# Kernel tuning notes

Measured on AMD Instinct MI355X. Metric: run time of the kernel, lower is better.

## Reference

```python
import jax, jax.numpy as jnp
import numpy as np

DIM_MODEL = 512
HEADS = 8
DIM_HEAD = 64
HIDDEN = HEADS * DIM_HEAD
SCALE = DIM_HEAD ** -0.5
GN_EPS = 1e-5


def setup_inputs() -> dict:
    key = jax.random.key(0)
    ks = jax.random.split(key, 7)
    b, t = 8, 4096
    x = jax.random.normal(ks[0], (b, DIM_MODEL, t), dtype=jnp.float32)
    mask = jax.random.randint(ks[1], (b, t), 0, 2) == 1  # bool padding mask
    # 1x1 convs are plain channel matmuls; kernels squeezed to 2D
    w_qkv = jax.random.normal(ks[2], (3 * HIDDEN, DIM_MODEL), dtype=jnp.float32) * (DIM_MODEL ** -0.5)
    w_out = jax.random.normal(ks[3], (DIM_MODEL, HIDDEN), dtype=jnp.float32) * (HIDDEN ** -0.5)
    b_out = jax.random.normal(ks[4], (DIM_MODEL,), dtype=jnp.float32) * 0.01
    gn_gamma = jnp.ones((DIM_MODEL,), dtype=jnp.float32)
    gn_beta = jnp.zeros((DIM_MODEL,), dtype=jnp.float32)
    return {"x": x, "mask": mask, "w_qkv": w_qkv, "w_out": w_out,
            "b_out": b_out, "gn_gamma": gn_gamma, "gn_beta": gn_beta}


def reference(x, mask, w_qkv, w_out, b_out, gn_gamma, gn_beta):
    b, c, t = x.shape
    # to_qkv: 1x1 conv == channel matmul -> [b, 3*hidden, t]
    qkv = jnp.einsum('oc,bct->bot', w_qkv, x)
    q, k, v = jnp.split(qkv, 3, axis=1)
    # 'b (h d) t -> b h d t'
    q = q.reshape(b, HEADS, DIM_HEAD, t)
    k = k.reshape(b, HEADS, DIM_HEAD, t)
    v = v.reshape(b, HEADS, DIM_HEAD, t)
    # additive mask: 0.0 where True, 1e-12 where False; broadcast 'b t -> b 1 1 t'
    maskf = jnp.where(mask, 0.0, 1e-12)[:, None, None, :].astype(x.dtype)
    q = jax.nn.softmax(q, axis=-2) * SCALE            # softmax over feature dim d
    k = jax.nn.softmax(k + maskf, axis=-1)            # softmax over time dim t
    # linear attention: O(t * d * e)
    context = jnp.einsum('bhdn,bhen->bhde', k, v)      # [b, h, d, e]
    out = jnp.einsum('bhde,bhdn->bhen', context, q)    # [b, h, e, t]
    out = out.reshape(b, HIDDEN, t)                    # 'b h e t -> b (h e) t'
    # to_out: 1x1 conv with bias, then GroupNorm(1, dim_model)
    y = jnp.einsum('oc,bct->bot', w_out, out) + b_out[None, :, None]
    mu = jnp.mean(y, axis=(1, 2), keepdims=True)
    var = jnp.var(y, axis=(1, 2), keepdims=True)
    y = (y - mu) * jax.lax.rsqrt(var + GN_EPS)
    return y * gn_gamma[None, :, None] + gn_beta[None, :, None]
```

## Files before the change

kernel.cpp:

```cpp
#include <hip/hip_runtime.h>
#include <stdint.h>

typedef unsigned short u16;
using f32x4 = __attribute__((ext_vector_type(4))) float;
using s16x8 = __attribute__((ext_vector_type(8))) short;

#define MFMA_BF16(a, b, c) __builtin_amdgcn_mfma_f32_16x16x32_bf16((a), (b), (c), 0, 0, 0)

#define GLOAD_LDS16(gptr, lptr)                                                               \
  __builtin_amdgcn_global_load_lds((const __attribute__((address_space(1))) uint32_t*)(gptr), \
                                   (__attribute__((address_space(3))) uint32_t*)(lptr), 16, 0, 0)

__device__ __forceinline__ u16 f2bf(float f) {
  union { float f; uint32_t u; } v; v.f = f;
  uint32_t r = v.u + 0x7fffu + ((v.u >> 16) & 1u);
  return (u16)(r >> 16);
}
__device__ __forceinline__ float bf2f(u16 h) {
  union { uint32_t u; float f; } v; v.u = ((uint32_t)h) << 16;
  return v.f;
}

__global__ void k_transpose_x(const float* __restrict__ x, u16* __restrict__ xT,
                              const float* __restrict__ wq, const float* __restrict__ wo,
                              u16* __restrict__ wqb, u16* __restrict__ wob) {
  if (blockIdx.z == 8) {
    const int nq = 1536 * 512 / 4;
    const int no = 512 * 512 / 4;
    int bid = blockIdx.y * 64 + blockIdx.x;
#pragma unroll
    for (int rep = 0; rep < 2; ++rep) {
      int i = bid * 256 + threadIdx.x + rep * 131072;
      if (i < nq) {
        float4 v = ((const float4*)wq)[i];
        u16* o = wqb + i * 4;
        o[0] = f2bf(v.x); o[1] = f2bf(v.y); o[2] = f2bf(v.z); o[3] = f2bf(v.w);
      } else if (i < nq + no) {
        int j = i - nq;
        float4 v = ((const float4*)wo)[j];
        u16* o = wob + j * 4;
        o[0] = f2bf(v.x); o[1] = f2bf(v.y); o[2] = f2bf(v.z); o[3] = f2bf(v.w);
      }
    }
    return;
  }
  __shared__ u16 tile[64][68];
  int b = blockIdx.z, c0 = blockIdx.y * 64, t0 = blockIdx.x * 64;
  const float* xp = x + ((size_t)b * 512 + c0) * 4096 + t0;
#pragma unroll
  for (int it = 0; it < 4; ++it) {
    int r = it * 16 + (threadIdx.x >> 4), c4 = (threadIdx.x & 15) * 4;
    float4 v = *(const float4*)(xp + (size_t)r * 4096 + c4);
    tile[r][c4 + 0] = f2bf(v.x);
    tile[r][c4 + 1] = f2bf(v.y);
    tile[r][c4 + 2] = f2bf(v.z);
    tile[r][c4 + 3] = f2bf(v.w);
  }
  __syncthreads();
  u16* op = xT + ((size_t)b * 4096 + t0) * 512 + c0;
#pragma unroll
  for (int it = 0; it < 2; ++it) {
    int tr = it * 32 + (threadIdx.x >> 3), cb = (threadIdx.x & 7) * 8;
    s16x8 o;
#pragma unroll
    for (int jj = 0; jj < 8; ++jj) o[jj] = tile[cb + jj][tr];
    *(s16x8*)(op + (size_t)tr * 512 + cb) = o;
  }
}

#define STAGE_A16(u, ktile, bf)                                                        \
  { int L = (u)*512 + tid; int r = L >> 3, pc = L & 7; int lc = pc ^ (r & 7);          \
    GLOAD_LDS16(Ab + (size_t)r * 512 + (ktile) * 64 + lc * 8,                          \
                ((char*)AL) + (bf) * 32768 + (size_t)L * 16); }
#define STAGE_B16(u, ktile, bf)                                                        \
  { int L = (u)*512 + tid; int r = L >> 3, pc = L & 7; int lc = pc ^ (r & 7);          \
    GLOAD_LDS16(BSRCX(r, ktile, lc),                                                   \
                ((char*)BL) + (bf) * 32768 + (size_t)L * 16); }

#define GEMM256_CORE()                                                                 \
  s16x8* AL = (s16x8*)lds;                                                             \
  s16x8* BL = (s16x8*)(lds + 65536);                                                   \
  int tid = threadIdx.x, w = tid >> 6, lane = tid & 63;                                \
  int wr = w >> 2, wc = w & 3;                                                         \
  int hi = lane >> 4, lo = lane & 15;                                                  \
  f32x4 acc[8][4] = {};                                                                \
  _Pragma("unroll")                                                                    \
  for (int u = 0; u < 4; ++u) STAGE_A16(u, 0, 0);                                      \
  _Pragma("unroll")                                                                    \
  for (int u = 0; u < 4; ++u) STAGE_B16(u, 0, 0);                                      \
  asm volatile("s_waitcnt vmcnt(0)" ::: "memory");                                     \
  __syncthreads();                                                                     \
  int cur = 0;                                                                         \
  _Pragma("unroll 2")                                                                  \
  for (int kt = 0; kt < 8; ++kt) {                                                     \
    const s16x8* Ac = AL + cur * 2048;                                                 \
    const s16x8* Bc = BL + cur * 2048;                                                 \
    int nxt = cur ^ 1;                                                                 \
    bool pf = (kt < 7);                                                                \
    s16x8 af[4][2], b0[2][2], b1[2][2];                                                \
    _Pragma("unroll")                                                                  \
    for (int mi = 0; mi < 4; ++mi) {                                                   \
      int r = wr * 128 + mi * 16 + lo;                                                 \
      _Pragma("unroll")                                                                \
      for (int kk = 0; kk < 2; ++kk) {                                                 \
        int lc = kk * 4 + hi;                                                          \
        af[mi][kk] = Ac[r * 8 + (lc ^ (r & 7))];                                       \
      }                                                                                \
    }                                                                                  \
    _Pragma("unroll")                                                                  \
    for (int ni = 0; ni < 2; ++ni) {                                                   \
      int r = wc * 64 + ni * 16 + lo;                                                  \
      _Pragma("unroll")                                                                \
      for (int kk = 0; kk < 2; ++kk) {                                                 \
        int lc = kk * 4 + hi;                                                          \
        b0[ni][kk] = Bc[r * 8 + (lc ^ (r & 7))];                                       \
      }                                                                                \
    }                                                                                  \
    if (pf) { STAGE_A16(0, kt + 1, nxt); STAGE_A16(1, kt + 1, nxt); }                  \
    __builtin_amdgcn_s_setprio(1);                                                     \
    _Pragma("unroll")                                                                  \
    for (int mi = 0; mi < 4; ++mi)                                                     \
      _Pragma("unroll")                                                                \
      for (int ni = 0; ni < 2; ++ni)                                                   \
        _Pragma("unroll")                                                              \
        for (int kk = 0; kk < 2; ++kk)                                                 \
          acc[mi][ni] = MFMA_BF16(af[mi][kk], b0[ni][kk], acc[mi][ni]);                \
    __builtin_amdgcn_s_setprio(0);                                                     \
    _Pragma("unroll")                                                                  \
    for (int ni = 0; ni < 2; ++ni) {                                                   \
      int r = wc * 64 + (ni + 2) * 16 + lo;                                            \
      _Pragma("unroll")                                                                \
      for (int kk = 0; kk < 2; ++kk) {                                                 \
        int lc = kk * 4 + hi;                                                          \
        b1[ni][kk] = Bc[r * 8 + (lc ^ (r & 7))];                                       \
      }                                                                                \
    }                                                                                  \
    if (pf) { STAGE_A16(2, kt + 1, nxt); STAGE_A16(3, kt + 1, nxt); }                  \
    __builtin_amdgcn_s_setprio(1);                                                     \
    _Pragma("unroll")                                                                  \
    for (int mi = 0; mi < 4; ++mi)                                                     \
      _Pragma("unroll")                                                                \
      for (int ni = 0; ni < 2; ++ni)                                                   \
        _Pragma("unroll")                                                              \
        for (int kk = 0; kk < 2; ++kk)                                                 \
          acc[mi][ni + 2] = MFMA_BF16(af[mi][kk], b1[ni][kk], acc[mi][ni + 2]);        \
    __builtin_amdgcn_s_setprio(0);                                                     \
    _Pragma("unroll")                                                                  \
    for (int mi = 0; mi < 4; ++mi) {                                                   \
      int r = wr * 128 + 64 + mi * 16 + lo;                                            \
      _Pragma("unroll")                                                                \
      for (int kk = 0; kk < 2; ++kk) {                                                 \
        int lc = kk * 4 + hi;                                                          \
        af[mi][kk] = Ac[r * 8 + (lc ^ (r & 7))];                                       \
      }                                                                                \
    }                                                                                  \
    if (pf) { STAGE_B16(0, kt + 1, nxt); STAGE_B16(1, kt + 1, nxt); }                  \
    __builtin_amdgcn_s_setprio(1);                                                     \
    _Pragma("unroll")                                                                  \
    for (int mi = 0; mi < 4; ++mi)                                                     \
      _Pragma("unroll")                                                                \
      for (int ni = 0; ni < 2; ++ni)                                                   \
        _Pragma("unroll")                                                              \
        for (int kk = 0; kk < 2; ++kk)                                                 \
          acc[mi + 4][ni + 2] = MFMA_BF16(af[mi][kk], b1[ni][kk], acc[mi + 4][ni + 2]);\
    __builtin_amdgcn_s_setprio(0);                                                     \
    if (pf) { STAGE_B16(2, kt + 1, nxt); STAGE_B16(3, kt + 1, nxt); }                  \
    __builtin_amdgcn_s_setprio(1);                                                     \
    _Pragma("unroll")                                                                  \
    for (int mi = 0; mi < 4; ++mi)                                                     \
      _Pragma("unroll")                                                                \
      for (int ni = 0; ni < 2; ++ni)                                                   \
        _Pragma("unroll")                                                              \
        for (int kk = 0; kk < 2; ++kk)                                                 \
          acc[mi + 4][ni] = MFMA_BF16(af[mi][kk], b0[ni][kk], acc[mi + 4][ni]);        \
    __builtin_amdgcn_s_setprio(0);                                                     \
    asm volatile("s_waitcnt vmcnt(0)" ::: "memory");                                   \
    __syncthreads();                                                                   \
    cur = nxt;                                                                         \
  }

#define BSRCX(r, ktile, lc) (Bb + (size_t)(r) * 512 + (ktile) * 64 + (lc) * 8)
__launch_bounds__(512, 2)
__global__ void k_gemm_qkv(const u16* __restrict__ A, const u16* __restrict__ BT,
                           u16* __restrict__ C, u16* __restrict__ qT,
                           float* __restrict__ spart) {
  extern __shared__ char lds[];
  int b = blockIdx.z;
  int m0 = blockIdx.y * 256, n0 = blockIdx.x * 256;
  const u16* Ab = A + (size_t)m0 * 512;
  const u16* Bb = BT + ((size_t)b * 4096 + n0) * 512;
  GEMM256_CORE()
  if (blockIdx.y < 2) {
#pragma unroll
    for (int hb = 0; hb < 2; ++hb) {
      int head = (int)blockIdx.y * 4 + wr * 2 + hb;
      int bh = b * 8 + head;
#pragma unroll
      for (int ni = 0; ni < 4; ++ni) {
        float mx = -1e30f;
#pragma unroll
        for (int mi = 0; mi < 4; ++mi)
#pragma unroll
          for (int j = 0; j < 4; ++j) mx = fmaxf(mx, acc[hb * 4 + mi][ni][j]);
        mx = fmaxf(mx, __shfl_xor(mx, 16));
        mx = fmaxf(mx, __shfl_xor(mx, 32));
        float e[4][4];
        float s = 0.f;
#pragma unroll
        for (int mi = 0; mi < 4; ++mi)
#pragma unroll
          for (int j = 0; j < 4; ++j) {
            e[mi][j] = __expf(acc[hb * 4 + mi][ni][j] - mx);
            s += e[mi][j];
          }
        s += __shfl_xor(s, 16);
        s += __shfl_xor(s, 32);
        float sc = 0.125f / s;
        int t = n0 + wc * 64 + ni * 16 + lo;
        u16* op = qT + ((size_t)bh * 4096 + t) * 64 + hi * 4;
#pragma unroll
        for (int mi = 0; mi < 4; ++mi) {
          union { u16 u[4]; uint2 v; } pk;
#pragma unroll
          for (int j = 0; j < 4; ++j) pk.u[j] = f2bf(e[mi][j] * sc);
          *(uint2*)(op + mi * 16) = pk.v;
        }
      }
    }
  } else if (blockIdx.y < 4) {
    u16* Cb = C + ((size_t)b * 1536 + m0) * 4096 + n0;
    float* ks = (float*)(lds + 131072);
#pragma unroll
    for (int mi = 0; mi < 8; ++mi)
#pragma unroll
      for (int j = 0; j < 4; ++j) {
        int mr = wr * 128 + mi * 16 + hi * 4 + j;
        float t = 0.f;
#pragma unroll
        for (int ni = 0; ni < 4; ++ni) {
          int nn = wc * 64 + ni * 16 + lo;
          float e = __expf(acc[mi][ni][j]);
          t += e;
          Cb[(size_t)mr * 4096 + nn] = f2bf(e);
        }
        t += __shfl_xor(t, 1);
        t += __shfl_xor(t, 2);
        t += __shfl_xor(t, 4);
        t += __shfl_xor(t, 8);
        if (lo == 0) ks[wc * 256 + mr] = t;
      }
    __syncthreads();
    if (tid < 256) {
      float v = ks[tid] + ks[256 + tid] + ks[512 + tid] + ks[768 + tid];
      spart[((size_t)b * 512 + (m0 - 512) + tid) * 16 + blockIdx.x] = v;
    }
  } else {
    u16* Cb = C + ((size_t)b * 1536 + m0) * 4096 + n0;
#pragma unroll
    for (int mi = 0; mi < 8; ++mi)
#pragma unroll
      for (int ni = 0; ni < 4; ++ni)
#pragma unroll
        for (int j = 0; j < 4; ++j) {
          int mr = wr * 128 + mi * 16 + hi * 4 + j;
          int nn = wc * 64 + ni * 16 + lo;
          Cb[(size_t)mr * 4096 + nn] = f2bf(acc[mi][ni][j]);
        }
  }
}
#undef BSRCX

#define BSRCX(r, ktile, lc) \
  (qTb + ((size_t)(((ktile) * 8 + (lc)) >> 3) * 4096 + n0 + (r)) * 64 + (((ktile) * 8 + (lc)) & 7) * 8)
__launch_bounds__(512, 2)
__global__ void k_gemm_final(const u16* __restrict__ Wf, const u16* __restrict__ qT,
                             u16* __restrict__ Ybf, const float* __restrict__ bias,
                             float2* __restrict__ part2) {
  extern __shared__ char lds[];
  int b = blockIdx.z;
  int m0 = blockIdx.y * 256, n0 = blockIdx.x * 256;
  const u16* Ab = Wf + ((size_t)b * 512 + m0) * 512;
  const u16* qTb = qT + (size_t)b * 8 * 4096 * 64;
  GEMM256_CORE()
  u16* Yb = Ybf + ((size_t)b * 512 + m0) * 4096 + n0;
  float sm = 0.f, ssm = 0.f;
#pragma unroll
  for (int mi = 0; mi < 8; ++mi)
#pragma unroll
    for (int j = 0; j < 4; ++j) {
      int mr = wr * 128 + mi * 16 + hi * 4 + j;
      float bo = bias[m0 + mr];
#pragma unroll
      for (int ni = 0; ni < 4; ++ni) {
        int nn = wc * 64 + ni * 16 + lo;
        float vv = acc[mi][ni][j] + bo;
        sm += vv;
        ssm += vv * vv;
        Yb[(size_t)mr * 4096 + nn] = f2bf(vv);
      }
    }
#pragma unroll
  for (int off = 32; off; off >>= 1) { sm += __shfl_xor(sm, off); ssm += __shfl_xor(ssm, off); }
  float* sr = (float*)lds;
  if (lane == 0) { sr[w] = sm; sr[8 + w] = ssm; }
  __syncthreads();
  if (tid == 0) {
    float2 o;
    o.x = 0.f; o.y = 0.f;
#pragma unroll
    for (int i = 0; i < 8; ++i) { o.x += sr[i]; o.y += sr[8 + i]; }
    part2[((size_t)b * 2 + blockIdx.y) * 16 + blockIdx.x] = o;
  }
}
#undef BSRCX

__global__ void k_context_part(const u16* __restrict__ qkv, float* __restrict__ ctxp) {
  int s = blockIdx.x, bh = blockIdx.y;
  int b = bh >> 3, h = bh & 7;
  int w = threadIdx.x >> 6, lane = threadIdx.x & 63;
  int hi = lane >> 4, lo = lane & 15;
  const u16* vb = qkv + ((size_t)b * 1536 + 1024 + h * 64) * 4096 + s * 256;
  const u16* kb = qkv + ((size_t)b * 1536 + 512 + h * 64) * 4096 + s * 256;
  int d = w * 16 + lo;
  f32x4 acc[4] = {};
#pragma unroll
  for (int st = 0; st < 8; ++st) {
    int nn = st * 32 + hi * 8;
    s16x8 bexp = *(const s16x8*)(kb + (size_t)d * 4096 + nn);
#pragma unroll
    for (int ei = 0; ei < 4; ++ei) {
      s16x8 a = *(const s16x8*)(vb + (size_t)(ei * 16 + lo) * 4096 + nn);
      acc[ei] = MFMA_BF16(a, bexp, acc[ei]);
    }
  }
  float* cp = ctxp + ((size_t)bh * 16 + s) * 4096;
#pragma unroll
  for (int ei = 0; ei < 4; ++ei) {
    float4 o;
    o.x = acc[ei][0]; o.y = acc[ei][1]; o.z = acc[ei][2]; o.w = acc[ei][3];
    *(float4*)&cp[(size_t)d * 64 + ei * 16 + hi * 4] = o;
  }
}

__global__ void k_ctx_reduce(const float* __restrict__ ctxp, const float* __restrict__ spart,
                             u16* __restrict__ Bg) {
  int q = blockIdx.x, bh = blockIdx.y;
  int b = bh >> 3, h = bh & 7;
  __shared__ float sinv[4];
  int tid = threadIdx.x;
  if (tid < 4) {
    int hd = h * 64 + q * 4 + tid;
    const float* sp = spart + ((size_t)b * 512 + hd) * 16;
    float s = 0.f;
#pragma unroll
    for (int xx = 0; xx < 16; ++xx) s += sp[xx];
    sinv[tid] = 1.f / s;
  }
  __syncthreads();
  int pos = q * 256 + tid;
  float v = 0.f;
#pragma unroll
  for (int si = 0; si < 16; ++si) v += ctxp[((size_t)bh * 16 + si) * 4096 + pos];
  Bg[(size_t)bh * 4096 + pos] = f2bf(v * sinv[(pos >> 6) & 3]);
}

__global__ void k_wfused(const u16* __restrict__ wout, const u16* __restrict__ Bg,
                         u16* __restrict__ Wf) {
  int bh = blockIdx.x;
  int b = bh >> 3, h = bh & 7;
  int w = threadIdx.x >> 6, lane = threadIdx.x & 63;
  int hi = lane >> 4, lo = lane & 15;
  const u16* Bb = Bg + (size_t)bh * 4096;
  const u16* Ab = wout + (size_t)h * 64;
  f32x4 acc[8][4] = {};
#pragma unroll
  for (int ks = 0; ks < 2; ++ks) {
    s16x8 bfr[4];
#pragma unroll
    for (int ni = 0; ni < 4; ++ni)
      bfr[ni] = *(const s16x8*)(Bb + (size_t)(ni * 16 + lo) * 64 + ks * 32 + hi * 8);
#pragma unroll
    for (int mi = 0; mi < 8; ++mi) {
      s16x8 a = *(const s16x8*)(Ab + (size_t)(w * 128 + mi * 16 + lo) * 512 + ks * 32 + hi * 8);
#pragma unroll
      for (int ni = 0; ni < 4; ++ni) acc[mi][ni] = MFMA_BF16(a, bfr[ni], acc[mi][ni]);
    }
  }
#pragma unroll
  for (int mi = 0; mi < 8; ++mi)
#pragma unroll
    for (int ni = 0; ni < 4; ++ni) {
      int m = w * 128 + mi * 16 + hi * 4;
      int d = ni * 16 + lo;
#pragma unroll
      for (int j = 0; j < 4; ++j)
        Wf[((size_t)b * 512 + m + j) * 512 + h * 64 + d] = f2bf(acc[mi][ni][j]);
    }
}

__global__ void k_gn_norm(const u16* __restrict__ ybf, float* __restrict__ y,
                          const float2* __restrict__ part2,
                          const float* __restrict__ gamma, const float* __restrict__ beta) {
  int b = blockIdx.y;
  float s = 0.f, ss = 0.f;
#pragma unroll
  for (int i = 0; i < 32; ++i) { float2 pp = part2[b * 32 + i]; s += pp.x; ss += pp.y; }
  const float N = 512.f * 4096.f;
  float mu = s / N;
  float var = ss / N - mu * mu;
  float rstd = rsqrtf(var + 1e-5f);
  size_t base = ((size_t)b << 21) + (size_t)blockIdx.x * 16384;
  const s16x8* ip = (const s16x8*)(ybf + base);
  float4* opf = (float4*)(y + base);
#pragma unroll
  for (int i = 0; i < 8; ++i) {
    int idx = threadIdx.x + i * 256;
    int loc = (int)(blockIdx.x * 16384) + idx * 8;
    int c = loc >> 12;
    float g = gamma[c] * rstd, bt = beta[c];
    s16x8 v = ip[idx];
    float4 o0, o1;
    o0.x = (bf2f((u16)v[0]) - mu) * g + bt;
    o0.y = (bf2f((u16)v[1]) - mu) * g + bt;
    o0.z = (bf2f((u16)v[2]) - mu) * g + bt;
    o0.w = (bf2f((u16)v[3]) - mu) * g + bt;
    o1.x = (bf2f((u16)v[4]) - mu) * g + bt;
    o1.y = (bf2f((u16)v[5]) - mu) * g + bt;
    o1.z = (bf2f((u16)v[6]) - mu) * g + bt;
    o1.w = (bf2f((u16)v[7]) - mu) * g + bt;
    opf[idx * 2] = o0;
    opf[idx * 2 + 1] = o1;
  }
}

extern "C" void kernel_launch(void* const* d_in, const int* in_sizes, int n_in,
                              void* d_out, int out_size, void* d_ws, size_t ws_size,
                              hipStream_t stream) {
  const float* x     = (const float*)d_in[0];
  const float* wqkv  = (const float*)d_in[2];
  const float* wout  = (const float*)d_in[3];
  const float* bout  = (const float*)d_in[4];
  const float* gamma = (const float*)d_in[5];
  const float* beta  = (const float*)d_in[6];
  float* y = (float*)d_out;

  char* ws = (char*)d_ws;
  u16*    qkv_b = (u16*)ws;
  u16*    ybf   = (u16*)ws;
  u16*    xT    = (u16*)(ws + 100663296);
  float*  ctxp  = (float*)(ws + 100663296);
  u16*    Bg    = (u16*)(ws + 117702656);
  u16*    qT    = (u16*)(ws + 134217728);
  u16*    wqkvb = (u16*)(ws + 167772160);
  u16*    woutb = (u16*)(ws + 169345024);
  u16*    Wfused= (u16*)(ws + 169869312);
  float2* part2 = (float2*)(ws + 174063616);
  float*  spart = (float*)(ws + 174071808);

  const int GEMM_LDS = 135168;
  (void)hipFuncSetAttribute((const void*)k_gemm_qkv,
                            hipFuncAttributeMaxDynamicSharedMemorySize, GEMM_LDS);
  (void)hipFuncSetAttribute((const void*)k_gemm_final,
                            hipFuncAttributeMaxDynamicSharedMemorySize, GEMM_LDS);

  {
    dim3 g(64, 8, 9);
    k_transpose_x<<<g, 256, 0, stream>>>(x, xT, wqkv, wout, wqkvb, woutb);
  }
  {
    dim3 g(16, 6, 8);
    k_gemm_qkv<<<g, 512, GEMM_LDS, stream>>>(wqkvb, xT, qkv_b, qT, spart);
  }
  {
    dim3 g(16, 64);
    k_context_part<<<g, 256, 0, stream>>>(qkv_b, ctxp);
  }
  {
    dim3 g(16, 64);
    k_ctx_reduce<<<g, 256, 0, stream>>>(ctxp, spart, Bg);
  }
  k_wfused<<<64, 256, 0, stream>>>(woutb, Bg, Wfused);
  {
    dim3 g(16, 2, 8);
    k_gemm_final<<<g, 512, GEMM_LDS, stream>>>(Wfused, qT, ybf, bout, part2);
  }
  {
    dim3 g(128, 8);
    k_gn_norm<<<g, 256, 0, stream>>>(ybf, y, part2, gamma, beta);
  }
}
```

Measured before the change: 167.6 us.

## Fuse context reduction into Wfused kernel and halve context split count

The context partial kernel now covers 512 time steps per block with 8 splits instead of 16, which halves the partial buffer and the reduction work. The separate reduce kernel is merged into the Wfused kernel: each block sums the 8 partials, applies the softmax normaliser and stages the bf16 context tile in padded LDS, then runs the MFMA product with W_out. This drops one launch and the global round trip through Bg. In exchange the context kernel has fewer blocks (512) and longer serial loops, and the fused kernel runs only 64 blocks that each do all the reduction work.

```diff
diff --git a/kernel.cpp b/kernel.cpp
--- a/kernel.cpp
+++ b/kernel.cpp
@@ -319,12 +319,12 @@
   int b = bh >> 3, h = bh & 7;
   int w = threadIdx.x >> 6, lane = threadIdx.x & 63;
   int hi = lane >> 4, lo = lane & 15;
-  const u16* vb = qkv + ((size_t)b * 1536 + 1024 + h * 64) * 4096 + s * 256;
-  const u16* kb = qkv + ((size_t)b * 1536 + 512 + h * 64) * 4096 + s * 256;
+  const u16* vb = qkv + ((size_t)b * 1536 + 1024 + h * 64) * 4096 + s * 512;
+  const u16* kb = qkv + ((size_t)b * 1536 + 512 + h * 64) * 4096 + s * 512;
   int d = w * 16 + lo;
   f32x4 acc[4] = {};
 #pragma unroll
-  for (int st = 0; st < 8; ++st) {
+  for (int st = 0; st < 16; ++st) {
     int nn = st * 32 + hi * 8;
     s16x8 bexp = *(const s16x8*)(kb + (size_t)d * 4096 + nn);
 #pragma unroll
@@ -333,7 +333,7 @@
       acc[ei] = MFMA_BF16(a, bexp, acc[ei]);
     }
   }
-  float* cp = ctxp + ((size_t)bh * 16 + s) * 4096;
+  float* cp = ctxp + ((size_t)bh * 8 + s) * 4096;
 #pragma unroll
   for (int ei = 0; ei < 4; ++ei) {
     float4 o;
@@ -342,35 +342,33 @@
   }
 }
 
-__global__ void k_ctx_reduce(const float* __restrict__ ctxp, const float* __restrict__ spart,
-                             u16* __restrict__ Bg) {
-  int q = blockIdx.x, bh = blockIdx.y;
+__global__ void k_ctx_wfused(const float* __restrict__ ctxp, const float* __restrict__ spart,
+                             const u16* __restrict__ wout, u16* __restrict__ Wf) {
+  __shared__ float sinv[64];
+  __shared__ __align__(16) u16 Bgl[64 * 72];
+  int bh = blockIdx.x;
   int b = bh >> 3, h = bh & 7;
-  __shared__ float sinv[4];
   int tid = threadIdx.x;
-  if (tid < 4) {
-    int hd = h * 64 + q * 4 + tid;
-    const float* sp = spart + ((size_t)b * 512 + hd) * 16;
+  if (tid < 64) {
+    const float* sp = spart + ((size_t)b * 512 + h * 64 + tid) * 16;
     float s = 0.f;
 #pragma unroll
     for (int xx = 0; xx < 16; ++xx) s += sp[xx];
     sinv[tid] = 1.f / s;
   }
   __syncthreads();
-  int pos = q * 256 + tid;
-  float v = 0.f;
-#pragma unroll
-  for (int si = 0; si < 16; ++si) v += ctxp[((size_t)bh * 16 + si) * 4096 + pos];
-  Bg[(size_t)bh * 4096 + pos] = f2bf(v * sinv[(pos >> 6) & 3]);
-}
-
-__global__ void k_wfused(const u16* __restrict__ wout, const u16* __restrict__ Bg,
-                         u16* __restrict__ Wf) {
-  int bh = blockIdx.x;
-  int b = bh >> 3, h = bh & 7;
-  int w = threadIdx.x >> 6, lane = threadIdx.x & 63;
-  int hi = lane >> 4, lo = lane & 15;
-  const u16* Bb = Bg + (size_t)bh * 4096;
+  const float* cb = ctxp + (size_t)bh * 8 * 4096;
+#pragma unroll
+  for (int i = 0; i < 16; ++i) {
+    int pos = i * 256 + tid;
+    float v = 0.f;
+#pragma unroll
+    for (int s8 = 0; s8 < 8; ++s8) v += cb[(size_t)s8 * 4096 + pos];
+    int d = pos >> 6, e = pos & 63;
+    Bgl[d * 72 + e] = f2bf(v * sinv[d]);
+  }
+  __syncthreads();
+  int w = tid >> 6, lane = tid & 63, hi = lane >> 4, lo = lane & 15;
   const u16* Ab = wout + (size_t)h * 64;
   f32x4 acc[8][4] = {};
 #pragma unroll
@@ -378,7 +376,7 @@
     s16x8 bfr[4];
 #pragma unroll
     for (int ni = 0; ni < 4; ++ni)
-      bfr[ni] = *(const s16x8*)(Bb + (size_t)(ni * 16 + lo) * 64 + ks * 32 + hi * 8);
+      bfr[ni] = *(const s16x8*)&Bgl[(ni * 16 + lo) * 72 + ks * 32 + hi * 8];
 #pragma unroll
     for (int mi = 0; mi < 8; ++mi) {
       s16x8 a = *(const s16x8*)(Ab + (size_t)(w * 128 + mi * 16 + lo) * 512 + ks * 32 + hi * 8);
@@ -449,7 +447,6 @@
   u16*    ybf   = (u16*)ws;
   u16*    xT    = (u16*)(ws + 100663296);
   float*  ctxp  = (float*)(ws + 100663296);
-  u16*    Bg    = (u16*)(ws + 117702656);
   u16*    qT    = (u16*)(ws + 134217728);
   u16*    wqkvb = (u16*)(ws + 167772160);
   u16*    woutb = (u16*)(ws + 169345024);
@@ -472,14 +469,10 @@
     k_gemm_qkv<<<g, 512, GEMM_LDS, stream>>>(wqkvb, xT, qkv_b, qT, spart);
   }
   {
-    dim3 g(16, 64);
+    dim3 g(8, 64);
     k_context_part<<<g, 256, 0, stream>>>(qkv_b, ctxp);
   }
-  {
-    dim3 g(16, 64);
-    k_ctx_reduce<<<g, 256, 0, stream>>>(ctxp, spart, Bg);
-  }
-  k_wfused<<<64, 256, 0, stream>>>(woutb, Bg, Wfused);
+  k_ctx_wfused<<<64, 256, 0, stream>>>(ctxp, spart, woutb, Wfused);
   {
     dim3 g(16, 2, 8);
     k_gemm_final<<<g, 512, GEMM_LDS, stream>>>(Wfused, qT, ybf, bout, part2);
```

New measurement: 186.7 us. 11.4% more time.

## Fuse GroupNorm into final GEMM with grid-wide per-batch atomic barrier

Applied to the files above, without the earlier changes.

The final GEMM now keeps biased outputs in registers, publishes per-block sum and sum-of-squares partials, and spins on a per-batch atomic counter until all 32 blocks of that batch arrive. It then applies the GroupNorm scale and shift and writes fp32 output directly. This removes the separate normalization kernel and the bf16 intermediate write and read of Y. It relies on all blocks being co-resident for the spin barrier and adds a counter memset and barrier wait time.

```diff
diff --git a/kernel.cpp b/kernel.cpp
--- a/kernel.cpp
+++ b/kernel.cpp
@@ -273,16 +273,17 @@
 #define BSRCX(r, ktile, lc) \
   (qTb + ((size_t)(((ktile) * 8 + (lc)) >> 3) * 4096 + n0 + (r)) * 64 + (((ktile) * 8 + (lc)) & 7) * 8)
 __launch_bounds__(512, 2)
-__global__ void k_gemm_final(const u16* __restrict__ Wf, const u16* __restrict__ qT,
-                             u16* __restrict__ Ybf, const float* __restrict__ bias,
-                             float2* __restrict__ part2) {
+__global__ void k_gemm_final_gn(const u16* __restrict__ Wf, const u16* __restrict__ qT,
+                                float* __restrict__ Y, const float* __restrict__ bias,
+                                float* __restrict__ part2, unsigned int* __restrict__ cnt,
+                                const float* __restrict__ gamma,
+                                const float* __restrict__ beta) {
   extern __shared__ char lds[];
   int b = blockIdx.z;
   int m0 = blockIdx.y * 256, n0 = blockIdx.x * 256;
   const u16* Ab = Wf + ((size_t)b * 512 + m0) * 512;
   const u16* qTb = qT + (size_t)b * 8 * 4096 * 64;
   GEMM256_CORE()
-  u16* Yb = Ybf + ((size_t)b * 512 + m0) * 4096 + n0;
   float sm = 0.f, ssm = 0.f;
 #pragma unroll
   for (int mi = 0; mi < 8; ++mi)
@@ -292,11 +293,10 @@
       float bo = bias[m0 + mr];
 #pragma unroll
       for (int ni = 0; ni < 4; ++ni) {
-        int nn = wc * 64 + ni * 16 + lo;
         float vv = acc[mi][ni][j] + bo;
+        acc[mi][ni][j] = vv;
         sm += vv;
         ssm += vv * vv;
-        Yb[(size_t)mr * 4096 + nn] = f2bf(vv);
       }
     }
 #pragma unroll
@@ -305,12 +305,42 @@
   if (lane == 0) { sr[w] = sm; sr[8 + w] = ssm; }
   __syncthreads();
   if (tid == 0) {
-    float2 o;
-    o.x = 0.f; o.y = 0.f;
-#pragma unroll
-    for (int i = 0; i < 8; ++i) { o.x += sr[i]; o.y += sr[8 + i]; }
-    part2[((size_t)b * 2 + blockIdx.y) * 16 + blockIdx.x] = o;
-  }
+    float s0 = 0.f, s1 = 0.f;
+#pragma unroll
+    for (int i = 0; i < 8; ++i) { s0 += sr[i]; s1 += sr[8 + i]; }
+    float* pf = part2 + ((size_t)b * 32 + blockIdx.y * 16 + blockIdx.x) * 2;
+    __hip_atomic_store(pf, s0, __ATOMIC_RELAXED, __HIP_MEMORY_SCOPE_AGENT);
+    __hip_atomic_store(pf + 1, s1, __ATOMIC_RELEASE, __HIP_MEMORY_SCOPE_AGENT);
+    __hip_atomic_fetch_add(&cnt[b], 1u, __ATOMIC_RELEASE, __HIP_MEMORY_SCOPE_AGENT);
+    while (__hip_atomic_load(&cnt[b], __ATOMIC_ACQUIRE, __HIP_MEMORY_SCOPE_AGENT) < 32u)
+      __builtin_amdgcn_s_sleep(2);
+  }
+  __syncthreads();
+  if (tid < 64) {
+    const float* pb = part2 + (size_t)b * 64;
+    sr[tid] = __hip_atomic_load(pb + tid, __ATOMIC_RELAXED, __HIP_MEMORY_SCOPE_AGENT);
+  }
+  __syncthreads();
+  float s = 0.f, ss = 0.f;
+#pragma unroll
+  for (int i = 0; i < 32; ++i) { s += sr[2 * i]; ss += sr[2 * i + 1]; }
+  const float N = 512.f * 4096.f;
+  float mu = s / N;
+  float var = ss / N - mu * mu;
+  float rstd = rsqrtf(var + 1e-5f);
+  float* Yb = Y + ((size_t)b * 512 + m0) * 4096 + n0;
+#pragma unroll
+  for (int mi = 0; mi < 8; ++mi)
+#pragma unroll
+    for (int j = 0; j < 4; ++j) {
+      int mr = wr * 128 + mi * 16 + hi * 4 + j;
+      float g = gamma[m0 + mr] * rstd, bt = beta[m0 + mr];
+#pragma unroll
+      for (int ni = 0; ni < 4; ++ni) {
+        int nn = wc * 64 + ni * 16 + lo;
+        Yb[(size_t)mr * 4096 + nn] = (acc[mi][ni][j] - mu) * g + bt;
+      }
+    }
 }
 #undef BSRCX
 
@@ -398,41 +428,6 @@
     }
 }
 
-__global__ void k_gn_norm(const u16* __restrict__ ybf, float* __restrict__ y,
-                          const float2* __restrict__ part2,
-                          const float* __restrict__ gamma, const float* __restrict__ beta) {
-  int b = blockIdx.y;
-  float s = 0.f, ss = 0.f;
-#pragma unroll
-  for (int i = 0; i < 32; ++i) { float2 pp = part2[b * 32 + i]; s += pp.x; ss += pp.y; }
-  const float N = 512.f * 4096.f;
-  float mu = s / N;
-  float var = ss / N - mu * mu;
-  float rstd = rsqrtf(var + 1e-5f);
-  size_t base = ((size_t)b << 21) + (size_t)blockIdx.x * 16384;
-  const s16x8* ip = (const s16x8*)(ybf + base);
-  float4* opf = (float4*)(y + base);
-#pragma unroll
-  for (int i = 0; i < 8; ++i) {
-    int idx = threadIdx.x + i * 256;
-    int loc = (int)(blockIdx.x * 16384) + idx * 8;
-    int c = loc >> 12;
-    float g = gamma[c] * rstd, bt = beta[c];
-    s16x8 v = ip[idx];
-    float4 o0, o1;
-    o0.x = (bf2f((u16)v[0]) - mu) * g + bt;
-    o0.y = (bf2f((u16)v[1]) - mu) * g + bt;
-    o0.z = (bf2f((u16)v[2]) - mu) * g + bt;
-    o0.w = (bf2f((u16)v[3]) - mu) * g + bt;
-    o1.x = (bf2f((u16)v[4]) - mu) * g + bt;
-    o1.y = (bf2f((u16)v[5]) - mu) * g + bt;
-    o1.z = (bf2f((u16)v[6]) - mu) * g + bt;
-    o1.w = (bf2f((u16)v[7]) - mu) * g + bt;
-    opf[idx * 2] = o0;
-    opf[idx * 2 + 1] = o1;
-  }
-}
-
 extern "C" void kernel_launch(void* const* d_in, const int* in_sizes, int n_in,
                               void* d_out, int out_size, void* d_ws, size_t ws_size,
                               hipStream_t stream) {
@@ -446,7 +441,6 @@
 
   char* ws = (char*)d_ws;
   u16*    qkv_b = (u16*)ws;
-  u16*    ybf   = (u16*)ws;
   u16*    xT    = (u16*)(ws + 100663296);
   float*  ctxp  = (float*)(ws + 100663296);
   u16*    Bg    = (u16*)(ws + 117702656);
@@ -454,13 +448,16 @@
   u16*    wqkvb = (u16*)(ws + 167772160);
   u16*    woutb = (u16*)(ws + 169345024);
   u16*    Wfused= (u16*)(ws + 169869312);
-  float2* part2 = (float2*)(ws + 174063616);
+  float*  part2 = (float*)(ws + 174063616);
   float*  spart = (float*)(ws + 174071808);
+  unsigned int* cnt = (unsigned int*)(ws + 174333952);
+
+  (void)hipMemsetAsync(cnt, 0, 32, stream);
 
   const int GEMM_LDS = 135168;
   (void)hipFuncSetAttribute((const void*)k_gemm_qkv,
                             hipFuncAttributeMaxDynamicSharedMemorySize, GEMM_LDS);
-  (void)hipFuncSetAttribute((const void*)k_gemm_final,
+  (void)hipFuncSetAttribute((const void*)k_gemm_final_gn,
                             hipFuncAttributeMaxDynamicSharedMemorySize, GEMM_LDS);
 
   {
@@ -482,10 +479,7 @@
   k_wfused<<<64, 256, 0, stream>>>(woutb, Bg, Wfused);
   {
     dim3 g(16, 2, 8);
-    k_gemm_final<<<g, 512, GEMM_LDS, stream>>>(Wfused, qT, ybf, bout, part2);
-  }
-  {
-    dim3 g(128, 8);
-    k_gn_norm<<<g, 256, 0, stream>>>(ybf, y, part2, gamma, beta);
-  }
-}
+    k_gemm_final_gn<<<g, 512, GEMM_LDS, stream>>>(Wfused, qT, y, bout, part2, cnt,
+                                                  gamma, beta);
+  }
+}
```

Result: no change. 170.5 us (+1.7%).
